# Kernel optimization log

Measured on AMD Instinct MI355X. Metric: run time of the kernel, lower is better.

## Reference

```python
import math
import jax, jax.numpy as jnp
import numpy as np

N_HEAD = 16

def setup_inputs() -> dict:
    key = jax.random.key(0)
    ks = jax.random.split(key, 3)
    B, T, C = 2, 2048, 1024
    x = jax.random.normal(ks[0], (B, T, C), dtype=jnp.float32)
    W_kqv = jax.random.normal(ks[1], (3 * C, C), dtype=jnp.float32) * 0.02
    b_kqv = jnp.zeros((3 * C,), dtype=jnp.float32)
    W_proj = jax.random.normal(ks[2], (C, C), dtype=jnp.float32) * 0.02
    b_proj = jnp.zeros((C,), dtype=jnp.float32)
    return {"x": x, "W_kqv": W_kqv, "b_kqv": b_kqv, "W_proj": W_proj, "b_proj": b_proj}

def reference(x, W_kqv, b_kqv, W_proj, b_proj):
    B, T, C = x.shape
    nh = N_HEAD
    hd = C // nh
    # fused QKV projection, then view [B,T,nh,3*hd] and slice into k,q,v
    kqv = (x @ W_kqv.T + b_kqv).reshape(B, T, nh, 3, hd)
    k = kqv[..., 0, :]  # [B,T,nh,hd]
    q = kqv[..., 1, :]
    v = kqv[..., 2, :]
    scale = 1.0 / math.sqrt(hd)
    att = jnp.einsum("bthd,bshd->bhts", q, k) * scale  # [B,nh,T,T]
    causal = jnp.tril(jnp.ones((T, T), dtype=bool))
    att = jnp.where(causal[None, None], att, -jnp.inf)
    att = jax.nn.softmax(att, axis=-1)
    y = jnp.einsum("bhts,bshd->bthd", att, v).reshape(B, T, C)
    return y @ W_proj.T + b_proj
```

## Files before the change

kernel.cpp:

```cpp
#include <hip/hip_runtime.h>

#define TSEQ 2048
#define NHEAD 16
#define HD 64
#define CDIM 1024
#define BT 4096

typedef unsigned short u16;
typedef __bf16 bf16x8 __attribute__((ext_vector_type(8)));
typedef float f32x4 __attribute__((ext_vector_type(4)));
typedef float f32x16 __attribute__((ext_vector_type(16)));

union Frag {
  int4 i4;
  bf16x8 b;
  u16 u[8];
};

__device__ __forceinline__ u16 f2b(float f) {
  union { float f; unsigned u; } x;
  x.f = f;
  unsigned r = x.u + 0x7fffu + ((x.u >> 16) & 1u);
  return (u16)(r >> 16);
}

#define N4X 1048576
#define N4W1 786432
#define N4W2 262144
__global__ void cvt3_kernel(const float* __restrict__ x, const float* __restrict__ w1,
                            const float* __restrict__ w2, u16* __restrict__ ox,
                            u16* __restrict__ o1, u16* __restrict__ o2) {
  int i = blockIdx.x * blockDim.x + threadIdx.x;
  int stride = gridDim.x * blockDim.x;
  for (int idx = i; idx < N4X + N4W1 + N4W2; idx += stride) {
    const float4* src;
    ushort4* dst;
    int k;
    if (idx < N4X) { src = (const float4*)x; dst = (ushort4*)ox; k = idx; }
    else if (idx < N4X + N4W1) { src = (const float4*)w1; dst = (ushort4*)o1; k = idx - N4X; }
    else { src = (const float4*)w2; dst = (ushort4*)o2; k = idx - N4X - N4W1; }
    float4 f = src[k];
    ushort4 o;
    o.x = f2b(f.x); o.y = f2b(f.y); o.z = f2b(f.z); o.w = f2b(f.w);
    dst[k] = o;
  }
}

__device__ __forceinline__ void gload_lds16(const u16* g, u16* l) {
  __builtin_amdgcn_global_load_lds((__attribute__((address_space(1))) void*)g,
                                   (__attribute__((address_space(3))) void*)l, 16, 0, 0);
}

__global__ __launch_bounds__(512, 2) void gemm_kqv(const u16* __restrict__ xb, const u16* __restrict__ wb,
                                                   const float* __restrict__ bias,
                                                   u16* __restrict__ qb, u16* __restrict__ kb,
                                                   u16* __restrict__ vtb) {
  __shared__ __align__(16) u16 SM[65536];

  const int tid = threadIdx.x;
  const int lane = tid & 63;
  const int wid = tid >> 6;
  const int wr = wid >> 2;
  const int wc = wid & 3;
  const int lr = lane & 15;
  const int hi = lane >> 4;
  const int frg = (hi ^ ((lr >> 1) & 3)) << 3;

  const int m0 = blockIdx.y * 128, n0 = blockIdx.x * 384;

  f32x4 acc[4][6];
#pragma unroll
  for (int i = 0; i < 4; i++)
#pragma unroll
    for (int j = 0; j < 6; j++) acc[i][j] = (f32x4){0.f, 0.f, 0.f, 0.f};

#define STG(b, jt, p)                                                                 \
  {                                                                                   \
    const size_t ko = (size_t)(jt) * 64 + (p) * 32;                                   \
    u16* Ad = SM + (b) * 32768 + (p) * 4096;                                          \
    u16* Bd = SM + (b) * 32768 + 8192 + (p) * 12288;                                  \
    { int c = tid; int row = c >> 2, c16 = c & 3;                                     \
      gload_lds16(&xb[(size_t)(m0 + row) * CDIM + ko + ((c16 ^ ((row >> 1) & 3)) << 3)], \
                  &Ad[c * 8]); }                                                      \
    _Pragma("unroll") for (int s = 0; s < 3; s++) {                                   \
      int c = tid + s * 512; int row = c >> 2, c16 = c & 3;                           \
      gload_lds16(&wb[(size_t)(n0 + row) * CDIM + ko + ((c16 ^ ((row >> 1) & 3)) << 3)], \
                  &Bd[c * 8]); }                                                      \
  }

  STG(0, 0, 0)
  STG(0, 0, 1)
  for (int jt = 0; jt < 16; ++jt) {
    const int bsel = jt & 1;
#pragma unroll
    for (int p = 0; p < 2; ++p) {
      if (jt == 15 && p == 1) asm volatile("s_waitcnt vmcnt(0)" ::: "memory");
      else                    asm volatile("s_waitcnt vmcnt(4)" ::: "memory");
      __builtin_amdgcn_s_barrier();
      const u16* Ap = SM + bsel * 32768 + p * 4096;
      const u16* Bp = SM + bsel * 32768 + 8192 + p * 12288;
      Frag af[4], bf[6];
#pragma unroll
      for (int mf = 0; mf < 4; mf++)
        af[mf].i4 = *(const int4*)&Ap[(wr * 64 + mf * 16 + lr) * 32 + frg];
#pragma unroll
      for (int nf = 0; nf < 6; nf++)
        bf[nf].i4 = *(const int4*)&Bp[(wc * 96 + nf * 16 + lr) * 32 + frg];
      __builtin_amdgcn_sched_barrier(0);
      if (jt + 1 < 16) STG((jt + 1) & 1, jt + 1, p)
      __builtin_amdgcn_sched_barrier(0);
      __builtin_amdgcn_s_setprio(1);
#pragma unroll
      for (int mf = 0; mf < 4; mf++)
#pragma unroll
        for (int nf = 0; nf < 6; nf++)
          acc[mf][nf] = __builtin_amdgcn_mfma_f32_16x16x32_bf16(af[mf].b, bf[nf].b, acc[mf][nf], 0, 0, 0);
      __builtin_amdgcn_s_setprio(0);
    }
  }
#undef STG

  __syncthreads();
  u16* Csh = SM;
  const int rbase = hi << 2;
#pragma unroll
  for (int mf = 0; mf < 4; mf++) {
#pragma unroll
    for (int nf = 0; nf < 6; nf++) {
      f32x4 a = acc[mf][nf];
      int nl = wc * 96 + nf * 16 + lr;
      int n = n0 + nl;
      float bval = bias[n];
      int sres = ((wc * 96 + nf * 16) % 192) >> 6;
      float scale = (sres == 1) ? 0.125f : 1.f;
#pragma unroll
      for (int r = 0; r < 4; r++) {
        int ml = wr * 64 + mf * 16 + rbase + r;
        Csh[ml * 384 + (nl ^ (((ml >> 2) & 3) << 4))] = f2b((a[r] + bval) * scale);
      }
    }
  }
  __syncthreads();

  const int bb = m0 >> 11, tt = m0 & 2047;
#pragma unroll
  for (int j = 0; j < 6; j++) {
    int sres = j % 3;
    int h = 2 * blockIdx.x + j / 3;
    int bh2 = (bb << 4) + h;
    if (sres == 2) {
      int ch = tid & 15;
      int d0 = tid >> 4;
#pragma unroll
      for (int it = 0; it < 2; it++) {
        int d = d0 + it * 32;
        unsigned pk[4];
#pragma unroll
        for (int p = 0; p < 4; p++) {
          int c0 = ch * 8 + p * 2;
          int g0 = c0 >> 6, c6a = c0 & 63;
          int mA = g0 * 64 + ((c6a & 51) | ((c6a & 8) >> 1) | ((c6a & 4) << 1));
          int c1 = c0 + 1;
          int g1 = c1 >> 6, c6b = c1 & 63;
          int mB = g1 * 64 + ((c6b & 51) | ((c6b & 8) >> 1) | ((c6b & 4) << 1));
          unsigned lo = Csh[mA * 384 + ((j * 64 + d) ^ (((mA >> 2) & 3) << 4))];
          unsigned hi2 = Csh[mB * 384 + ((j * 64 + d) ^ (((mB >> 2) & 3) << 4))];
          pk[p] = lo | (hi2 << 16);
        }
        int4 v4; v4.x = pk[0]; v4.y = pk[1]; v4.z = pk[2]; v4.w = pk[3];
        *(int4*)&vtb[((size_t)bh2 * HD + d) * TSEQ + tt + ch * 8] = v4;
      }
    } else {
      u16* dst = (sres == 0) ? kb : qb;
      int ch = tid & 7;
      int rg = tid >> 3;
#pragma unroll
      for (int it = 0; it < 2; it++) {
        int m = rg + it * 64;
        int ccp = (j * 8 + ch) ^ (((m >> 2) & 3) << 1);
        int4 v4 = *(const int4*)&Csh[m * 384 + (ccp << 3)];
        *(int4*)&dst[((size_t)bh2 * TSEQ + tt + m) * HD + ch * 8] = v4;
      }
    }
  }
}

__device__ __forceinline__ void gemm_tiles64(const u16* __restrict__ A, const u16* __restrict__ Bw,
                                             int K, int m0, int n0,
                                             u16 (*__restrict__ Ash)[2048],
                                             u16 (*__restrict__ Bsh)[4096],
                                             f32x4 acc[2][4]) {
  const int tid = threadIdx.x;
  const int lane = tid & 63;
  const int w = tid >> 6;
  const int wr = (w >> 1) * 32, wc = (w & 1) * 64;
  const int lr = lane & 15;
  const int hi = lane >> 4;
  const int r0 = tid >> 2;
  const int cS = ((tid & 3) ^ ((tid >> 3) & 3)) << 3;
  const int frg = (hi ^ ((lr >> 1) & 3)) << 3;

#define GSTAGE64(B, KO)                                                               \
  {                                                                                   \
    gload_lds16(&A[(size_t)(m0 + r0) * K + (KO) + cS], &Ash[B][tid * 8]);             \
    _Pragma("unroll") for (int s = 0; s < 2; s++)                                     \
      gload_lds16(&Bw[(size_t)(n0 + s * 64 + r0) * K + (KO) + cS], &Bsh[B][(s * 256 + tid) * 8]); \
  }

  GSTAGE64(0, 0)
  int cur = 0;
  for (int k0 = 0; k0 < K; k0 += 32) {
    __syncthreads();
    Frag af[2], bfr[4];
#pragma unroll
    for (int i = 0; i < 2; i++)
      af[i].i4 = *(const int4*)&Ash[cur][(wr + i * 16 + lr) * 32 + frg];
#pragma unroll
    for (int i = 0; i < 4; i++)
      bfr[i].i4 = *(const int4*)&Bsh[cur][(wc + i * 16 + lr) * 32 + frg];
    __builtin_amdgcn_sched_barrier(0);
    if (k0 + 32 < K) GSTAGE64(cur ^ 1, k0 + 32)
    __builtin_amdgcn_sched_barrier(0);
#pragma unroll
    for (int mf = 0; mf < 2; mf++)
#pragma unroll
      for (int nf = 0; nf < 4; nf++)
        acc[mf][nf] = __builtin_amdgcn_mfma_f32_16x16x32_bf16(af[mf].b, bfr[nf].b, acc[mf][nf], 0, 0, 0);
    cur ^= 1;
  }
#undef GSTAGE64
}

__global__ __launch_bounds__(256) void gemm_proj(const u16* __restrict__ yb, const u16* __restrict__ wb,
                                                 const float* __restrict__ bias,
                                                 float* __restrict__ out) {
  __shared__ __align__(16) u16 Ash[2][2048];
  __shared__ __align__(16) u16 Bsh[2][4096];
  const int m0 = blockIdx.y * 64, n0 = blockIdx.x * 128;
  f32x4 acc[2][4];
#pragma unroll
  for (int i = 0; i < 2; i++)
#pragma unroll
    for (int j = 0; j < 4; j++) acc[i][j] = (f32x4){0.f, 0.f, 0.f, 0.f};

  gemm_tiles64(yb, wb, CDIM, m0, n0, Ash, Bsh, acc);

  const int tid = threadIdx.x;
  const int lane = tid & 63;
  const int w = tid >> 6;
  const int wr = (w >> 1) * 32, wc = (w & 1) * 64;
  const int lr = lane & 15;
  const int rbase = (lane >> 4) << 2;
#pragma unroll
  for (int mf = 0; mf < 2; mf++) {
#pragma unroll
    for (int nf = 0; nf < 4; nf++) {
      f32x4 a = acc[mf][nf];
      int n = n0 + wc + nf * 16 + lr;
      float bval = bias[n];
#pragma unroll
      for (int r = 0; r < 4; r++) {
        int m = m0 + wr + mf * 16 + rbase + r;
        out[(size_t)m * CDIM + n] = a[r] + bval;
      }
    }
  }
}

__global__ __launch_bounds__(256, 2) void attn_kernel(const u16* __restrict__ qb,
                                                      const u16* __restrict__ kb,
                                                      const u16* __restrict__ vtb,
                                                      u16* __restrict__ yb) {
  __shared__ u16 Ksh[2][128 * 64];
  __shared__ u16 Vsh[2][64 * 128];

  const int tid = threadIdx.x;
  const int lane = tid & 63;
  const int w = tid >> 6;
  const int l31 = lane & 31;
  const int hi32 = lane >> 5;
  const int swz = l31 & 7;

  const int jj = blockIdx.x;
  const int bh = jj & 31;
  const int cls = jj >> 5;
  const int qbk = (cls < 8) ? (15 - cls) : (cls - 8);
  const int q0w = qbk * 128 + w * 32;
  const int LN = qbk + 1;

  const u16* Qp = qb + (size_t)bh * TSEQ * HD;
  const u16* Kp = kb + (size_t)bh * TSEQ * HD;
  const u16* Vt = vtb + (size_t)bh * HD * TSEQ;

  Frag qf[4];
#pragma unroll
  for (int k = 0; k < 4; k++)
    qf[k].i4 = *(const int4*)&Qp[(size_t)(q0w + l31) * HD + k * 16 + hi32 * 8];

  f32x16 O0, O1;
  float lp = 0.f;
#pragma unroll
  for (int i = 0; i < 16; i++) { O0[i] = 0.f; O1[i] = 0.f; }

#define STAGE(B, JT)                                                                 \
  {                                                                                  \
    const int kvb = (JT) * 128;                                                      \
    _Pragma("unroll") for (int p = 0; p < 4; p++) {                                  \
      int c = tid + p * 256;                                                         \
      int row = c >> 3, c16 = c & 7;                                                 \
      gload_lds16(&Kp[(size_t)(kvb + row) * HD + ((c16 ^ (row & 7)) << 3)],          \
                  &Ksh[B][c * 8]);                                                   \
    }                                                                                \
    _Pragma("unroll") for (int p = 0; p < 4; p++) {                                  \
      int c = tid + p * 256;                                                         \
      int row = c >> 4, c16 = c & 15;                                                \
      int gofs = ((c16 >> 3) << 6) + (((c16 & 7) ^ (row & 7)) << 3);                 \
      gload_lds16(&Vt[(size_t)row * TSEQ + kvb + gofs], &Vsh[B][c * 8]);             \
    }                                                                                \
  }

#define PACK2(dst, SV, base)                                                         \
    asm("v_cvt_pk_bf16_f32 %0, %1, %2" : "=v"(dst.i4.x) : "v"(SV[base + 0]), "v"(SV[base + 1])); \
    asm("v_cvt_pk_bf16_f32 %0, %1, %2" : "=v"(dst.i4.y) : "v"(SV[base + 2]), "v"(SV[base + 3])); \
    asm("v_cvt_pk_bf16_f32 %0, %1, %2" : "=v"(dst.i4.z) : "v"(SV[base + 4]), "v"(SV[base + 5])); \
    asm("v_cvt_pk_bf16_f32 %0, %1, %2" : "=v"(dst.i4.w) : "v"(SV[base + 6]), "v"(SV[base + 7]));

  STAGE(0, 0)
  int cur = 0;
  for (int jt = 0; jt < LN; ++jt) {
    __syncthreads();
    const bool diag = (jt == LN - 1);
    const int wlim = diag ? w : 3;
    const u16* Kt = Ksh[cur];
    const u16* Vl = Vsh[cur];

    Frag ka[4][4], vA[4][2], vB[4][2];
#pragma unroll
    for (int sh = 0; sh < 4; ++sh) {
      if (sh <= wlim) {
#pragma unroll
        for (int k = 0; k < 4; ++k)
          ka[sh][k].i4 = *(const int4*)&Kt[(sh * 32 + l31) * 64 + (((2 * k + hi32) ^ swz) << 3)];
#pragma unroll
        for (int k = 0; k < 2; ++k) {
          int cofs = ((sh >> 1) << 6) + (((((sh & 1) << 2) + 2 * k + hi32) ^ swz) << 3);
          vA[sh][k].i4 = *(const int4*)&Vl[l31 * 128 + cofs];
          vB[sh][k].i4 = *(const int4*)&Vl[(32 + l31) * 128 + cofs];
        }
      }
    }
    __builtin_amdgcn_sched_barrier(0);
    if (jt + 1 < LN) STAGE(cur ^ 1, jt + 1)
    __builtin_amdgcn_sched_barrier(0);
#pragma unroll
    for (int sh = 0; sh < 4; ++sh) {
      if (sh <= wlim) {
        f32x16 S;
#pragma unroll
        for (int i = 0; i < 16; i++) S[i] = 0.f;
        __builtin_amdgcn_s_setprio(1);
#pragma unroll
        for (int k = 0; k < 4; k++)
          S = __builtin_amdgcn_mfma_f32_32x32x16_bf16(ka[sh][k].b, qf[k].b, S, 0, 0, 0);
        __builtin_amdgcn_s_setprio(0);
        if (diag && sh == w) {
#pragma unroll
          for (int reg = 0; reg < 16; reg++) {
            int crow = (reg & 3) + 8 * (reg >> 2) + 4 * hi32;
            S[reg] = (crow <= l31) ? __expf(S[reg]) : 0.f;
          }
        } else {
#pragma unroll
          for (int reg = 0; reg < 16; reg++) S[reg] = __expf(S[reg]);
        }
#pragma unroll
        for (int reg = 0; reg < 16; reg++) lp += S[reg];
        Frag pa[2];
        PACK2(pa[0], S, 0)
        PACK2(pa[1], S, 8)
        __builtin_amdgcn_s_setprio(1);
#pragma unroll
        for (int k = 0; k < 2; k++) {
          O0 = __builtin_amdgcn_mfma_f32_32x32x16_bf16(pa[k].b, vA[sh][k].b, O0, 0, 0, 0);
          O1 = __builtin_amdgcn_mfma_f32_32x32x16_bf16(pa[k].b, vB[sh][k].b, O1, 0, 0, 0);
        }
        __builtin_amdgcn_s_setprio(0);
      }
    }
    cur ^= 1;
  }
#undef STAGE
#undef PACK2

  float lpt = lp + __shfl_xor(lp, 32);
  const int b = bh >> 4, h = bh & 15;
#pragma unroll
  for (int reg = 0; reg < 16; reg++) {
    int qlocal = (reg & 3) + 8 * (reg >> 2) + 4 * hi32;
    float invr = 1.f / __shfl(lpt, qlocal);
    int t = q0w + qlocal;
    size_t rowoff = ((size_t)(b * TSEQ + t) << 10) + (h << 6);
    yb[rowoff + l31] = f2b(O0[reg] * invr);
    yb[rowoff + 32 + l31] = f2b(O1[reg] * invr);
  }
}

extern "C" void kernel_launch(void* const* d_in, const int* in_sizes, int n_in,
                              void* d_out, int out_size, void* d_ws, size_t ws_size,
                              hipStream_t stream) {
  const float* x = (const float*)d_in[0];
  const float* Wkqv = (const float*)d_in[1];
  const float* bkqv = (const float*)d_in[2];
  const float* Wproj = (const float*)d_in[3];
  const float* bproj = (const float*)d_in[4];
  float* out = (float*)d_out;

  u16* ws = (u16*)d_ws;
  u16* xb = ws;
  u16* wkqvb = xb + 4194304;
  u16* wprojb = wkqvb + 3145728;
  u16* qb = wprojb + 1048576;
  u16* kb = qb + 4194304;
  u16* vtb = kb + 4194304;
  u16* yb = vtb + 4194304;

  cvt3_kernel<<<2048, 256, 0, stream>>>(x, Wkqv, Wproj, xb, wkqvb, wprojb);
  gemm_kqv<<<dim3(8, 32), 512, 0, stream>>>(xb, wkqvb, bkqv, qb, kb, vtb);
  attn_kernel<<<512, 256, 0, stream>>>(qb, kb, vtb, yb);
  gemm_proj<<<dim3(8, 64), 256, 0, stream>>>(yb, wprojb, bproj, out);
}
```

Baseline: 89.97 us.

## Deepen QKV GEMM LDS pipeline to four stages and fold log2e into Q scale

The QKV projection GEMM main loop changes from double-buffered 64-wide k-tiles split into two halves to a four-slot ring of 32-wide k-slices, with three slices prefetched ahead. The vmcnt waits are adjusted to match, so global-to-LDS loads get more time in flight and there is one barrier per slice. Separately, the Q scaling now includes log2(e), which lets the attention kernel use exp2f instead of __expf and drop a multiply per exponential. LDS use stays the same (4×16384 elements versus 2×32768), but the deeper ring keeps more loads outstanding.

```diff
diff --git a/kernel.cpp b/kernel.cpp
--- a/kernel.cpp
+++ b/kernel.cpp
@@ -74,11 +74,11 @@
 #pragma unroll
     for (int j = 0; j < 6; j++) acc[i][j] = (f32x4){0.f, 0.f, 0.f, 0.f};
 
-#define STG(b, jt, p)                                                                 \
+#define STG(sl)                                                                       \
   {                                                                                   \
-    const size_t ko = (size_t)(jt) * 64 + (p) * 32;                                   \
-    u16* Ad = SM + (b) * 32768 + (p) * 4096;                                          \
-    u16* Bd = SM + (b) * 32768 + 8192 + (p) * 12288;                                  \
+    const size_t ko = (size_t)(sl) * 32;                                              \
+    u16* Ad = SM + ((sl) & 3) * 4096;                                                 \
+    u16* Bd = SM + 16384 + ((sl) & 3) * 12288;                                        \
     { int c = tid; int row = c >> 2, c16 = c & 3;                                     \
       gload_lds16(&xb[(size_t)(m0 + row) * CDIM + ko + ((c16 ^ ((row >> 1) & 3)) << 3)], \
                   &Ad[c * 8]); }                                                      \
@@ -88,35 +88,33 @@
                   &Bd[c * 8]); }                                                      \
   }
 
-  STG(0, 0, 0)
-  STG(0, 0, 1)
-  for (int jt = 0; jt < 16; ++jt) {
-    const int bsel = jt & 1;
-#pragma unroll
-    for (int p = 0; p < 2; ++p) {
-      if (jt == 15 && p == 1) asm volatile("s_waitcnt vmcnt(0)" ::: "memory");
-      else                    asm volatile("s_waitcnt vmcnt(4)" ::: "memory");
-      __builtin_amdgcn_s_barrier();
-      const u16* Ap = SM + bsel * 32768 + p * 4096;
-      const u16* Bp = SM + bsel * 32768 + 8192 + p * 12288;
-      Frag af[4], bf[6];
-#pragma unroll
-      for (int mf = 0; mf < 4; mf++)
-        af[mf].i4 = *(const int4*)&Ap[(wr * 64 + mf * 16 + lr) * 32 + frg];
+  STG(0)
+  STG(1)
+  STG(2)
+  for (int ph = 0; ph < 32; ++ph) {
+    if (ph < 30)       asm volatile("s_waitcnt vmcnt(8)" ::: "memory");
+    else if (ph == 30) asm volatile("s_waitcnt vmcnt(4)" ::: "memory");
+    else               asm volatile("s_waitcnt vmcnt(0)" ::: "memory");
+    __builtin_amdgcn_s_barrier();
+    const u16* Ap = SM + (ph & 3) * 4096;
+    const u16* Bp = SM + 16384 + (ph & 3) * 12288;
+    Frag af[4], bf[6];
+#pragma unroll
+    for (int mf = 0; mf < 4; mf++)
+      af[mf].i4 = *(const int4*)&Ap[(wr * 64 + mf * 16 + lr) * 32 + frg];
+#pragma unroll
+    for (int nf = 0; nf < 6; nf++)
+      bf[nf].i4 = *(const int4*)&Bp[(wc * 96 + nf * 16 + lr) * 32 + frg];
+    __builtin_amdgcn_sched_barrier(0);
+    if (ph + 3 < 32) STG(ph + 3)
+    __builtin_amdgcn_sched_barrier(0);
+    __builtin_amdgcn_s_setprio(1);
+#pragma unroll
+    for (int mf = 0; mf < 4; mf++)
 #pragma unroll
       for (int nf = 0; nf < 6; nf++)
-        bf[nf].i4 = *(const int4*)&Bp[(wc * 96 + nf * 16 + lr) * 32 + frg];
-      __builtin_amdgcn_sched_barrier(0);
-      if (jt + 1 < 16) STG((jt + 1) & 1, jt + 1, p)
-      __builtin_amdgcn_sched_barrier(0);
-      __builtin_amdgcn_s_setprio(1);
-#pragma unroll
-      for (int mf = 0; mf < 4; mf++)
-#pragma unroll
-        for (int nf = 0; nf < 6; nf++)
-          acc[mf][nf] = __builtin_amdgcn_mfma_f32_16x16x32_bf16(af[mf].b, bf[nf].b, acc[mf][nf], 0, 0, 0);
-      __builtin_amdgcn_s_setprio(0);
-    }
+        acc[mf][nf] = __builtin_amdgcn_mfma_f32_16x16x32_bf16(af[mf].b, bf[nf].b, acc[mf][nf], 0, 0, 0);
+    __builtin_amdgcn_s_setprio(0);
   }
 #undef STG
 
@@ -132,7 +130,7 @@
       int n = n0 + nl;
       float bval = bias[n];
       int sres = ((wc * 96 + nf * 16) % 192) >> 6;
-      float scale = (sres == 1) ? 0.125f : 1.f;
+      float scale = (sres == 1) ? 0.125f * 1.4426950408889634f : 1.f;
 #pragma unroll
       for (int r = 0; r < 4; r++) {
         int ml = wr * 64 + mf * 16 + rbase + r;
@@ -367,11 +365,11 @@
 #pragma unroll
           for (int reg = 0; reg < 16; reg++) {
             int crow = (reg & 3) + 8 * (reg >> 2) + 4 * hi32;
-            S[reg] = (crow <= l31) ? __expf(S[reg]) : 0.f;
+            S[reg] = (crow <= l31) ? exp2f(S[reg]) : 0.f;
           }
         } else {
 #pragma unroll
-          for (int reg = 0; reg < 16; reg++) S[reg] = __expf(S[reg]);
+          for (int reg = 0; reg < 16; reg++) S[reg] = exp2f(S[reg]);
         }
 #pragma unroll
         for (int reg = 0; reg < 16; reg++) lp += S[reg];
```

Result: slower. 96.99 us (+7.8%).

## Split attention KV tiles across warp pairs with 64-row query blocks

Applied to the files above, without the earlier changes.

The attention kernel now uses 64-row query blocks and 64-key tiles. The four warps form two pairs: each pair shares 32 query rows and each warp in a pair handles half of every key tile. The two partial outputs and row sums are merged through shared memory at the end. Shared memory is halved, the launch bound is raised to four blocks per SM, and the grid doubles to 1024 blocks with a new causal load-balancing order. The goal is more parallelism and occupancy and finer causal skipping, paid for with an extra reduction step and sync and more per-tile overhead.

```diff
diff --git a/kernel.cpp b/kernel.cpp
--- a/kernel.cpp
+++ b/kernel.cpp
@@ -267,16 +267,19 @@
   }
 }
 
-__global__ __launch_bounds__(256, 2) void attn_kernel(const u16* __restrict__ qb,
+__global__ __launch_bounds__(256, 4) void attn_kernel(const u16* __restrict__ qb,
                                                       const u16* __restrict__ kb,
                                                       const u16* __restrict__ vtb,
                                                       u16* __restrict__ yb) {
-  __shared__ u16 Ksh[2][128 * 64];
-  __shared__ u16 Vsh[2][64 * 128];
+  __shared__ __align__(16) u16 SMEM[16384];
+  u16* Ksh0 = SMEM;
+  u16* Vsh0 = SMEM + 8192;
 
   const int tid = threadIdx.x;
   const int lane = tid & 63;
   const int w = tid >> 6;
+  const int u = w >> 1;
+  const int p = w & 1;
   const int l31 = lane & 31;
   const int hi32 = lane >> 5;
   const int swz = l31 & 7;
@@ -284,9 +287,11 @@
   const int jj = blockIdx.x;
   const int bh = jj & 31;
   const int cls = jj >> 5;
-  const int qbk = (cls < 8) ? (15 - cls) : (cls - 8);
-  const int q0w = qbk * 128 + w * 32;
-  const int LN = qbk + 1;
+  const int a = cls & 7, sel = cls >> 3;
+  const int qs = (sel == 0) ? 31 - a : (sel == 1) ? 16 + a : (sel == 2) ? 15 - a : a;
+  const int q0w = qs * 64 + u * 32;
+  const int LN = qs + 1;
+  const int qg = q0w + l31;
 
   const u16* Qp = qb + (size_t)bh * TSEQ * HD;
   const u16* Kp = kb + (size_t)bh * TSEQ * HD;
@@ -304,18 +309,13 @@
 
 #define STAGE(B, JT)                                                                 \
   {                                                                                  \
-    const int kvb = (JT) * 128;                                                      \
-    _Pragma("unroll") for (int p = 0; p < 4; p++) {                                  \
-      int c = tid + p * 256;                                                         \
+    const int kvb = (JT) * 64;                                                       \
+    _Pragma("unroll") for (int q_ = 0; q_ < 2; q_++) {                               \
+      int c = tid + q_ * 256;                                                        \
       int row = c >> 3, c16 = c & 7;                                                 \
-      gload_lds16(&Kp[(size_t)(kvb + row) * HD + ((c16 ^ (row & 7)) << 3)],          \
-                  &Ksh[B][c * 8]);                                                   \
-    }                                                                                \
-    _Pragma("unroll") for (int p = 0; p < 4; p++) {                                  \
-      int c = tid + p * 256;                                                         \
-      int row = c >> 4, c16 = c & 15;                                                \
-      int gofs = ((c16 >> 3) << 6) + (((c16 & 7) ^ (row & 7)) << 3);                 \
-      gload_lds16(&Vt[(size_t)row * TSEQ + kvb + gofs], &Vsh[B][c * 8]);             \
+      int gofs = (c16 ^ (row & 7)) << 3;                                             \
+      gload_lds16(&Kp[(size_t)(kvb + row) * HD + gofs], &Ksh0[(B) * 4096 + c * 8]);  \
+      gload_lds16(&Vt[(size_t)row * TSEQ + kvb + gofs], &Vsh0[(B) * 4096 + c * 8]);  \
     }                                                                                \
   }
 
@@ -329,63 +329,58 @@
   int cur = 0;
   for (int jt = 0; jt < LN; ++jt) {
     __syncthreads();
-    const bool diag = (jt == LN - 1);
-    const int wlim = diag ? w : 3;
-    const u16* Kt = Ksh[cur];
-    const u16* Vl = Vsh[cur];
-
-    Frag ka[4][4], vA[4][2], vB[4][2];
-#pragma unroll
-    for (int sh = 0; sh < 4; ++sh) {
-      if (sh <= wlim) {
-#pragma unroll
-        for (int k = 0; k < 4; ++k)
-          ka[sh][k].i4 = *(const int4*)&Kt[(sh * 32 + l31) * 64 + (((2 * k + hi32) ^ swz) << 3)];
-#pragma unroll
-        for (int k = 0; k < 2; ++k) {
-          int cofs = ((sh >> 1) << 6) + (((((sh & 1) << 2) + 2 * k + hi32) ^ swz) << 3);
-          vA[sh][k].i4 = *(const int4*)&Vl[l31 * 128 + cofs];
-          vB[sh][k].i4 = *(const int4*)&Vl[(32 + l31) * 128 + cofs];
-        }
+    const int kv0 = jt * 64 + p * 32;
+    const bool act = (kv0 <= q0w + 31);
+    const bool masked = act && (kv0 + 31 > q0w);
+    const u16* Kt = Ksh0 + cur * 4096;
+    const u16* Vl = Vsh0 + cur * 4096;
+
+    Frag ka[4], vA[2], vB[2];
+    if (act) {
+#pragma unroll
+      for (int k = 0; k < 4; ++k)
+        ka[k].i4 = *(const int4*)&Kt[(p * 32 + l31) * 64 + (((2 * k + hi32) ^ swz) << 3)];
+#pragma unroll
+      for (int k = 0; k < 2; ++k) {
+        int cofs = ((2 * (k + 2 * p) + hi32) ^ swz) << 3;
+        vA[k].i4 = *(const int4*)&Vl[l31 * 64 + cofs];
+        vB[k].i4 = *(const int4*)&Vl[(32 + l31) * 64 + cofs];
       }
     }
     __builtin_amdgcn_sched_barrier(0);
     if (jt + 1 < LN) STAGE(cur ^ 1, jt + 1)
     __builtin_amdgcn_sched_barrier(0);
-#pragma unroll
-    for (int sh = 0; sh < 4; ++sh) {
-      if (sh <= wlim) {
-        f32x16 S;
-#pragma unroll
-        for (int i = 0; i < 16; i++) S[i] = 0.f;
-        __builtin_amdgcn_s_setprio(1);
-#pragma unroll
-        for (int k = 0; k < 4; k++)
-          S = __builtin_amdgcn_mfma_f32_32x32x16_bf16(ka[sh][k].b, qf[k].b, S, 0, 0, 0);
-        __builtin_amdgcn_s_setprio(0);
-        if (diag && sh == w) {
-#pragma unroll
-          for (int reg = 0; reg < 16; reg++) {
-            int crow = (reg & 3) + 8 * (reg >> 2) + 4 * hi32;
-            S[reg] = (crow <= l31) ? __expf(S[reg]) : 0.f;
-          }
-        } else {
-#pragma unroll
-          for (int reg = 0; reg < 16; reg++) S[reg] = __expf(S[reg]);
+    if (act) {
+      f32x16 S;
+#pragma unroll
+      for (int i = 0; i < 16; i++) S[i] = 0.f;
+      __builtin_amdgcn_s_setprio(1);
+#pragma unroll
+      for (int k = 0; k < 4; k++)
+        S = __builtin_amdgcn_mfma_f32_32x32x16_bf16(ka[k].b, qf[k].b, S, 0, 0, 0);
+      __builtin_amdgcn_s_setprio(0);
+      if (masked) {
+#pragma unroll
+        for (int reg = 0; reg < 16; reg++) {
+          int crow = (reg & 3) + 8 * (reg >> 2) + 4 * hi32;
+          S[reg] = (kv0 + crow <= qg) ? __expf(S[reg]) : 0.f;
         }
-#pragma unroll
-        for (int reg = 0; reg < 16; reg++) lp += S[reg];
-        Frag pa[2];
-        PACK2(pa[0], S, 0)
-        PACK2(pa[1], S, 8)
-        __builtin_amdgcn_s_setprio(1);
-#pragma unroll
-        for (int k = 0; k < 2; k++) {
-          O0 = __builtin_amdgcn_mfma_f32_32x32x16_bf16(pa[k].b, vA[sh][k].b, O0, 0, 0, 0);
-          O1 = __builtin_amdgcn_mfma_f32_32x32x16_bf16(pa[k].b, vB[sh][k].b, O1, 0, 0, 0);
-        }
-        __builtin_amdgcn_s_setprio(0);
-      }
+      } else {
+#pragma unroll
+        for (int reg = 0; reg < 16; reg++) S[reg] = __expf(S[reg]);
+      }
+#pragma unroll
+      for (int reg = 0; reg < 16; reg++) lp += S[reg];
+      Frag pa[2];
+      PACK2(pa[0], S, 0)
+      PACK2(pa[1], S, 8)
+      __builtin_amdgcn_s_setprio(1);
+#pragma unroll
+      for (int k = 0; k < 2; k++) {
+        O0 = __builtin_amdgcn_mfma_f32_32x32x16_bf16(pa[k].b, vA[k].b, O0, 0, 0, 0);
+        O1 = __builtin_amdgcn_mfma_f32_32x32x16_bf16(pa[k].b, vB[k].b, O1, 0, 0, 0);
+      }
+      __builtin_amdgcn_s_setprio(0);
     }
     cur ^= 1;
   }
@@ -393,15 +388,31 @@
 #undef PACK2
 
   float lpt = lp + __shfl_xor(lp, 32);
-  const int b = bh >> 4, h = bh & 15;
-#pragma unroll
-  for (int reg = 0; reg < 16; reg++) {
-    int qlocal = (reg & 3) + 8 * (reg >> 2) + 4 * hi32;
-    float invr = 1.f / __shfl(lpt, qlocal);
-    int t = q0w + qlocal;
-    size_t rowoff = ((size_t)(b * TSEQ + t) << 10) + (h << 6);
-    yb[rowoff + l31] = f2b(O0[reg] * invr);
-    yb[rowoff + 32 + l31] = f2b(O1[reg] * invr);
+
+  __syncthreads();
+  float* Om = (float*)SMEM;
+  if (p == 1) {
+    float* dst = Om + (u * 64 + lane) * 33;
+#pragma unroll
+    for (int reg = 0; reg < 16; reg++) { dst[reg] = O0[reg]; dst[16 + reg] = O1[reg]; }
+    dst[32] = lpt;
+  }
+  __syncthreads();
+  if (p == 0) {
+    const float* src = Om + (u * 64 + lane) * 33;
+#pragma unroll
+    for (int reg = 0; reg < 16; reg++) { O0[reg] += src[reg]; O1[reg] += src[16 + reg]; }
+    float ltot = lpt + src[32];
+    const int b = bh >> 4, h = bh & 15;
+#pragma unroll
+    for (int reg = 0; reg < 16; reg++) {
+      int qlocal = (reg & 3) + 8 * (reg >> 2) + 4 * hi32;
+      float invr = 1.f / __shfl(ltot, qlocal);
+      int t = q0w + qlocal;
+      size_t rowoff = ((size_t)(b * TSEQ + t) << 10) + (h << 6);
+      yb[rowoff + l31] = f2b(O0[reg] * invr);
+      yb[rowoff + 32 + l31] = f2b(O1[reg] * invr);
+    }
   }
 }
 
@@ -426,6 +437,6 @@
 
   cvt3_kernel<<<2048, 256, 0, stream>>>(x, Wkqv, Wproj, xb, wkqvb, wprojb);
   gemm_kqv<<<dim3(8, 32), 512, 0, stream>>>(xb, wkqvb, bkqv, qb, kb, vtb);
-  attn_kernel<<<512, 256, 0, stream>>>(qb, kb, vtb, yb);
+  attn_kernel<<<1024, 256, 0, stream>>>(qb, kb, vtb, yb);
   gemm_proj<<<dim3(8, 64), 256, 0, stream>>>(yb, wprojb, bproj, out);
 }
```

Result: slower. 103.0 us (+14.5%).
